# Performance work log

Hardware: AMD Instinct MI355X
Metric: run time of the kernel (lower is better)

## Reference

```python
import jax, jax.numpy as jnp
import numpy as np

S, B, T = 2048, 256, 48


def setup_inputs() -> dict:
    key = jax.random.key(0)
    k1, k2, k3, k4 = jax.random.split(key, 4)
    emissions = jax.random.normal(k1, (S, B, T), dtype=jnp.float32)
    tags = jax.random.randint(k2, (S, B), 0, T, dtype=jnp.int64)
    mask = jnp.ones((S, B), dtype=jnp.int32)
    # params initialized uniform(-0.1, 0.1) as in reset_parameters
    start_transitions = jax.random.uniform(k3, (T,), minval=-0.1, maxval=0.1, dtype=jnp.float32)
    end_transitions = jax.random.uniform(k4, (T,), minval=-0.1, maxval=0.1, dtype=jnp.float32)
    transitions = jax.random.uniform(jax.random.fold_in(key, 7), (T, T), minval=-0.1, maxval=0.1, dtype=jnp.float32)
    return {
        "emissions": emissions,
        "tags": tags,
        "mask": mask,
        "start_transitions": start_transitions,
        "end_transitions": end_transitions,
        "transitions": transitions,
    }


def _compute_score(emissions, tags, mask, start_transitions, end_transitions, transitions):
    # emissions: (S,B,T), tags/mask: (S,B)
    seq_length, batch_size = tags.shape
    maskf = mask.astype(emissions.dtype)
    ar = jnp.arange(batch_size)
    # emission score of the chosen tag at every step: (S,B)
    em_scores = jnp.take_along_axis(emissions, tags[..., None], axis=2)[..., 0]
    score = start_transitions[tags[0]] + em_scores[0]
    # transition scores between consecutive tags, masked: (S-1,B)
    trans_scores = transitions[tags[:-1], tags[1:]] * maskf[1:]
    score = score + trans_scores.sum(axis=0) + (em_scores[1:] * maskf[1:]).sum(axis=0)
    seq_ends = mask.astype(jnp.int32).sum(axis=0) - 1  # (B,)
    last_tags = tags[seq_ends, ar]
    score = score + end_transitions[last_tags]
    return score  # (B,)


def _compute_normalizer(emissions, mask, start_transitions, end_transitions, transitions):
    # forward algorithm via lax.scan over time
    score0 = start_transitions + emissions[0]  # (B,T)

    def step(score, inp):
        em_i, m_i = inp  # (B,T), (B,)
        # (B, T_prev, T_next)
        next_score = jax.nn.logsumexp(score[:, :, None] + transitions[None, :, :] + em_i[:, None, :], axis=1)
        score = jnp.where(m_i[:, None] != 0, next_score, score)
        return score, None

    score, _ = jax.lax.scan(step, score0, (emissions[1:], mask[1:]))
    score = score + end_transitions
    return jax.nn.logsumexp(score, axis=1)  # (B,)


def reference(emissions, tags, mask, start_transitions, end_transitions, transitions):
    numerator = _compute_score(emissions, tags, mask, start_transitions, end_transitions, transitions)
    denominator = _compute_normalizer(emissions, mask, start_transitions, end_transitions, transitions)
    llh = numerator - denominator
    return llh.sum()  # reduction='sum'
```

## Files before the change

### kernel.cpp

```cpp
#include <hip/hip_runtime.h>
#include <hip/hip_bf16.h>
#include <math.h>

#define S_LEN  2048
#define B_SZ   256
#define T_TAGS 48
#define MAT_U32 1152

#define WS_CNT_OFF 0
#define WS_K_OFF   1024
#define WS_P_OFF   65536

using short8 = __attribute__((ext_vector_type(8))) short;
using f32x4  = __attribute__((ext_vector_type(4))) float;

__device__ __forceinline__ unsigned cvtpk(float lo, float hi) {
    unsigned r;
    asm("v_cvt_pk_bf16_f32 %0, %1, %2" : "=v"(r) : "v"(lo), "v"(hi));
    return r;
}
__device__ __forceinline__ unsigned pk2bf(float lo, float hi) {
    __hip_bfloat162 h2 = __float22bfloat162_rn(make_float2(lo, hi));
    return *reinterpret_cast<unsigned*>(&h2);
}

template<int CCH>
__global__ __launch_bounds__(64, 4) void crf_chunk_kernel(
    const float* __restrict__ em, const int* __restrict__ mask,
    const float* __restrict__ trans, const int* __restrict__ tags,
    const float* __restrict__ startT, unsigned* __restrict__ wsP,
    int* __restrict__ wsK, int* __restrict__ wsCnt, float* __restrict__ out)
{
    constexpr int LCH = S_LEN / CCH;
    constexpr int NQ  = LCH / 64;
    const int bid = blockIdx.x;
    const int b = bid / CCH, c = bid % CCH;
    const int tid = threadIdx.x;
    const int cc = tid & 15, g = tid >> 4;
    const int start = c * LCH;

    __shared__ __align__(16) uint4 lds4[384];
    char* Lc = (char*)lds4;

#pragma unroll
    for (int i = 0; i < 6; ++i) lds4[tid + 64 * i] = make_uint4(0u, 0u, 0u, 0u);
    __builtin_amdgcn_wave_barrier();
    if (tid < T_TAGS)
        *(unsigned short*)(Lc + (tid >> 4) * 2048 +
                           ((tid >> 3) * 16 + (tid & 15)) * 16 + (tid & 7) * 2) = 0x3F80;
    __builtin_amdgcn_wave_barrier();

    unsigned long long ball[NQ];
    int cnt = 0;
#pragma unroll
    for (int q = 0; q < NQ; ++q) {
        const int s = start + q * 64 + tid;
        ball[q] = __ballot(mask[s * B_SZ + b] != 0);
        cnt += (int)__popcll(ball[q]);
    }
    if (tid == 0) atomicAdd(&wsCnt[b], cnt);
    if (c == 0) ball[0] &= ~1ull;

    short8 Afr[3][2];
#pragma unroll
    for (int jt = 0; jt < 3; ++jt) {
        const int j = jt * 16 + cc;
#pragma unroll
        for (int kt = 0; kt < 2; ++kt) {
            unsigned u[4];
#pragma unroll
            for (int h = 0; h < 4; ++h) {
                const int k0 = kt * 32 + g * 8 + 2 * h;
                const float lo = (k0     < T_TAGS) ? __expf(trans[k0 * T_TAGS + j]) : 0.f;
                const float hi = (k0 + 1 < T_TAGS) ? __expf(trans[(k0 + 1) * T_TAGS + j]) : 0.f;
                u[h] = cvtpk(lo, hi);
            }
            uint4 uu = make_uint4(u[0], u[1], u[2], u[3]);
            Afr[jt][kt] = *reinterpret_cast<short8*>(&uu);
        }
    }

    int K = 0, pend = 0;
    float kf = 0.0f;
    const f32x4 fz = {0.f, 0.f, 0.f, 0.f};
    const size_t embase = (size_t)b * T_TAGS + 4 * g;

    auto emload = [&](int t, f32x4& d0, f32x4& d1, f32x4& d2) {
        int ss = start + t; if (ss > S_LEN - 1) ss = S_LEN - 1;
        const float* p = em + (size_t)ss * (B_SZ * T_TAGS) + embase;
        d0 = *(const f32x4*)(p);
        d1 = *(const f32x4*)(p + 16);
        d2 = *(const f32x4*)(p + 32);
    };

    auto step = [&](bool on, const f32x4& e0, const f32x4& e1, const f32x4& e2) {
        if (!on) return;
        const short8 B00 = *(const short8*)(Lc +        tid * 16);
        const short8 B01 = *(const short8*)(Lc + 1024 + tid * 16);
        const short8 B10 = *(const short8*)(Lc + 2048 + tid * 16);
        const short8 B11 = *(const short8*)(Lc + 3072 + tid * 16);
        const short8 B20 = *(const short8*)(Lc + 4096 + tid * 16);
        const short8 B21 = *(const short8*)(Lc + 5120 + tid * 16);
        const float kf_ = kf;
        constexpr float L2E = 1.4426950408889634f;
        float ef0[4], ef1[4], ef2[4];
#pragma unroll
        for (int r = 0; r < 4; ++r) {
            ef0[r] = exp2f(fmaf(e0[r], L2E, kf_));
            ef1[r] = exp2f(fmaf(e1[r], L2E, kf_));
            ef2[r] = exp2f(fmaf(e2[r], L2E, kf_));
        }
        f32x4 z;
#define DOFRAG(JT, NT, BN0, BN1, EF, PROBE_)                                   \
        z = __builtin_amdgcn_mfma_f32_16x16x32_bf16(Afr[JT][0], BN0, fz, 0, 0, 0); \
        z = __builtin_amdgcn_mfma_f32_16x16x32_bf16(Afr[JT][1], BN1, z,  0, 0, 0); \
        if (PROBE_) {                                                          \
            const unsigned pb_ = (unsigned)__builtin_amdgcn_readfirstlane(     \
                (int)__float_as_uint(z[0]));                                   \
            const int ee_ = (int)((pb_ >> 23) & 255u);                         \
            const int kk_ = ee_ - 127;                                         \
            K += kk_; pend = kk_;                                              \
            kf = (float)(-kk_);                                                \
        }                                                                      \
        *(uint2*)(Lc + (NT) * 2048 +                                           \
                  ((2 * (JT) + (g >> 1)) * 16 + cc) * 16 + (g & 1) * 8) =      \
            make_uint2(cvtpk(z[0] * EF[0], z[1] * EF[1]),                      \
                       cvtpk(z[2] * EF[2], z[3] * EF[3]))

        DOFRAG(0, 0, B00, B01, ef0, true);
        DOFRAG(0, 1, B10, B11, ef0, false);
        DOFRAG(0, 2, B20, B21, ef0, false);
        DOFRAG(1, 0, B00, B01, ef1, false);
        DOFRAG(1, 1, B10, B11, ef1, false);
        DOFRAG(1, 2, B20, B21, ef1, false);
        DOFRAG(2, 0, B00, B01, ef2, false);
        DOFRAG(2, 1, B10, B11, ef2, false);
        DOFRAG(2, 2, B20, B21, ef2, false);
#undef DOFRAG
    };

    f32x4 a0, a1, a2, b0, b1, b2;
    emload(0, a0, a1, a2);
    emload(1, b0, b1, b2);

#pragma unroll
    for (int q = 0; q < NQ; ++q) {
        const unsigned long long bq = ball[q];
        for (int tt = 0; tt < 64; tt += 2) {
            const int t = q * 64 + tt;
            step(((bq >> tt) & 1ull) != 0, a0, a1, a2);
            emload(t + 2, a0, a1, a2);
            step(((bq >> (tt + 1)) & 1ull) != 0, b0, b1, b2);
            emload(t + 3, b0, b1, b2);
        }
    }

    auto mkI = [&](int shift) -> short8 {
        const int e = cc + shift - 8 * g;
        uint4 uu;
        uu.x = (e == 0) ? 0x3F80u : (e == 1) ? 0x3F800000u : 0u;
        uu.y = (e == 2) ? 0x3F80u : (e == 3) ? 0x3F800000u : 0u;
        uu.z = (e == 4) ? 0x3F80u : (e == 5) ? 0x3F800000u : 0u;
        uu.w = (e == 6) ? 0x3F80u : (e == 7) ? 0x3F800000u : 0u;
        return *reinterpret_cast<short8*>(&uu);
    };
    const short8 I0  = mkI(0);
    const short8 I16 = mkI(16);

    short8 F0[3], F1[3];
#pragma unroll
    for (int nt = 0; nt < 3; ++nt) {
        F0[nt] = *(const short8*)(Lc + nt * 2048 +        tid * 16);
        F1[nt] = *(const short8*)(Lc + nt * 2048 + 1024 + tid * 16);
    }
#pragma unroll
    for (int nt = 0; nt < 3; ++nt) {
#pragma unroll
        for (int ct = 0; ct < 3; ++ct) {
            const short8 Af = (ct < 2) ? F0[nt] : F1[nt];
            const short8 Bi = (ct == 1) ? I16 : I0;
            f32x4 z = __builtin_amdgcn_mfma_f32_16x16x32_bf16(Af, Bi, fz, 0, 0, 0);
            const int jcol = ct * 16 + cc;
            *(uint2*)&wsP[(size_t)bid * MAT_U32 + jcol * 24 + nt * 8 + g * 2] =
                make_uint2(pk2bf(z[0], z[1]), pk2bf(z[2], z[3]));
        }
    }
    if (tid == 0) wsK[bid] = K - pend;

    {
        float nacc = 0.f;
#pragma unroll
        for (int q = 0; q < NQ; ++q) {
            const int s = start + q * 64 + tid;
            if (s == 0) {
                const int t0 = tags[b];
                nacc += em[(size_t)b * T_TAGS + t0] + startT[t0];
            } else if ((ball[q] >> tid) & 1ull) {
                const int tc = tags[(size_t)s * B_SZ + b];
                const int tp = tags[(size_t)(s - 1) * B_SZ + b];
                nacc += em[((size_t)s * B_SZ + b) * T_TAGS + tc] + trans[tp * T_TAGS + tc];
            }
        }
#pragma unroll
        for (int off = 32; off > 0; off >>= 1) nacc += __shfl_down(nacc, off);
        if (tid == 0) atomicAdd(out, nacc);
    }
}

template<int CCH>
__global__ __launch_bounds__(64, 1) void crf_combine_kernel(
    const float* __restrict__ em, const float* __restrict__ startT,
    const float* __restrict__ endT, const unsigned* __restrict__ wsP,
    const int* __restrict__ wsK, const int* __restrict__ wsCnt,
    const int* __restrict__ tags, float* __restrict__ out)
{
    const int b = blockIdx.x, tid = threadIdx.x;
    const int j = (tid < T_TAGS) ? tid : 0;
    float v = (tid < T_TAGS) ? __expf(startT[j] + em[(size_t)b * T_TAGS + j]) : 0.f;
    int K2 = 0;
    for (int c = 0; c < CCH; ++c) {
        const unsigned base = (unsigned)(b * CCH + c) * MAT_U32 + j * 24;
        uint4 W[6];
#pragma unroll
        for (int q = 0; q < 6; ++q)
            W[q] = *reinterpret_cast<const uint4*>(&wsP[base + 4 * q]);
        float a0 = 0.f, a1 = 0.f;
#pragma unroll
        for (int q = 0; q < 6; ++q) {
            const unsigned wv[4] = {W[q].x, W[q].y, W[q].z, W[q].w};
#pragma unroll
            for (int r = 0; r < 4; ++r) {
                const int i = q * 8 + r * 2;
                const float p0 = __uint_as_float(wv[r] << 16);
                const float p1 = __uint_as_float(wv[r] & 0xFFFF0000u);
                a0 = fmaf(__uint_as_float(__builtin_amdgcn_readlane(__float_as_uint(v), i)), p0, a0);
                a1 = fmaf(__uint_as_float(__builtin_amdgcn_readlane(__float_as_uint(v), i + 1)), p1, a1);
            }
        }
        const float vn = a0 + a1;
        const unsigned pb = (unsigned)__builtin_amdgcn_readfirstlane((int)__float_as_uint(vn));
        const int ee = (int)((pb >> 23) & 255u);
        const float sc = __uint_as_float((unsigned)(254 - ee) << 23);
        v = vn * sc;
        K2 += (ee - 127) + wsK[b * CCH + c];
    }
    float contrib = (tid < T_TAGS) ? v * __expf(endT[j]) : 0.f;
#pragma unroll
    for (int off = 32; off > 0; off >>= 1) contrib += __shfl_down(contrib, off);
    if (tid == 0) {
        const int cnt  = wsCnt[b];
        const int last = tags[(size_t)(cnt - 1) * B_SZ + b];
        const double den = (double)K2 * 0.6931471805599453 + (double)__logf(contrib);
        atomicAdd(out, endT[last] + (float)(-den));
    }
}

extern "C" void kernel_launch(void* const* d_in, const int* in_sizes, int n_in,
                              void* d_out, int out_size, void* d_ws, size_t ws_size,
                              hipStream_t stream)
{
    const float* em     = (const float*)d_in[0];
    const int*   tags   = (const int*)  d_in[1];
    const int*   mask   = (const int*)  d_in[2];
    const float* startT = (const float*)d_in[3];
    const float* endT   = (const float*)d_in[4];
    const float* trans  = (const float*)d_in[5];
    float* out = (float*)d_out;

    int*      wsCnt = (int*)((char*)d_ws + WS_CNT_OFF);
    int*      wsK   = (int*)((char*)d_ws + WS_K_OFF);
    unsigned* wsP   = (unsigned*)((char*)d_ws + WS_P_OFF);

    hipMemsetAsync(out, 0, sizeof(float), stream);
    hipMemsetAsync(wsCnt, 0, B_SZ * sizeof(int), stream);

    const size_t need16 = (size_t)WS_P_OFF + (size_t)(B_SZ * 16) * (MAT_U32 * 4);
    if (ws_size >= need16) {
        crf_chunk_kernel<16><<<B_SZ * 16, 64, 0, stream>>>(em, mask, trans, tags, startT, wsP, wsK, wsCnt, out);
        crf_combine_kernel<16><<<B_SZ, 64, 0, stream>>>(em, startT, endT, wsP, wsK, wsCnt, tags, out);
    } else {
        crf_chunk_kernel<8><<<B_SZ * 8, 64, 0, stream>>>(em, mask, trans, tags, startT, wsP, wsK, wsCnt, out);
        crf_combine_kernel<8><<<B_SZ, 64, 0, stream>>>(em, startT, endT, wsP, wsK, wsCnt, tags, out);
    }
}
```

Measured before the change: 227.4 us.

## Move numerator gather into combine kernel and pack scale math as float2

The gold-path score (numerator) gather and its per-block atomicAdd move out of the chunk kernel into the combine kernel. There, each of 256 blocks loops over the full sequence reading mask, tags, emissions and transitions. The emission scaling and bf16 conversion in the chunk step are rewritten with two-wide float vectors so the compiler can emit packed FMA/multiply instructions. This removes the scattered gathers and thousands of atomics from the critical chunk kernel, but serializes that work onto far fewer blocks in the combine kernel, where it may add latency.

```diff
diff --git a/kernel.cpp b/kernel.cpp
--- a/kernel.cpp
+++ b/kernel.cpp
@@ -13,6 +13,7 @@
 
 using short8 = __attribute__((ext_vector_type(8))) short;
 using f32x4  = __attribute__((ext_vector_type(4))) float;
+using f32x2  = __attribute__((ext_vector_type(2))) float;
 
 __device__ __forceinline__ unsigned cvtpk(float lo, float hi) {
     unsigned r;
@@ -27,9 +28,8 @@
 template<int CCH>
 __global__ __launch_bounds__(64, 4) void crf_chunk_kernel(
     const float* __restrict__ em, const int* __restrict__ mask,
-    const float* __restrict__ trans, const int* __restrict__ tags,
-    const float* __restrict__ startT, unsigned* __restrict__ wsP,
-    int* __restrict__ wsK, int* __restrict__ wsCnt, float* __restrict__ out)
+    const float* __restrict__ trans, unsigned* __restrict__ wsP,
+    int* __restrict__ wsK, int* __restrict__ wsCnt)
 {
     constexpr int LCH = S_LEN / CCH;
     constexpr int NQ  = LCH / 64;
@@ -101,17 +101,23 @@
         const short8 B11 = *(const short8*)(Lc + 3072 + tid * 16);
         const short8 B20 = *(const short8*)(Lc + 4096 + tid * 16);
         const short8 B21 = *(const short8*)(Lc + 5120 + tid * 16);
-        const float kf_ = kf;
         constexpr float L2E = 1.4426950408889634f;
-        float ef0[4], ef1[4], ef2[4];
-#pragma unroll
-        for (int r = 0; r < 4; ++r) {
-            ef0[r] = exp2f(fmaf(e0[r], L2E, kf_));
-            ef1[r] = exp2f(fmaf(e1[r], L2E, kf_));
-            ef2[r] = exp2f(fmaf(e2[r], L2E, kf_));
-        }
+        const f32x2 kf2 = {kf, kf};
+        const f32x2 l2e2 = {L2E, L2E};
+        f32x2 x0a = (f32x2){e0[0], e0[1]} * l2e2 + kf2;
+        f32x2 x0b = (f32x2){e0[2], e0[3]} * l2e2 + kf2;
+        f32x2 x1a = (f32x2){e1[0], e1[1]} * l2e2 + kf2;
+        f32x2 x1b = (f32x2){e1[2], e1[3]} * l2e2 + kf2;
+        f32x2 x2a = (f32x2){e2[0], e2[1]} * l2e2 + kf2;
+        f32x2 x2b = (f32x2){e2[2], e2[3]} * l2e2 + kf2;
+        const f32x2 ef0a = {exp2f(x0a[0]), exp2f(x0a[1])};
+        const f32x2 ef0b = {exp2f(x0b[0]), exp2f(x0b[1])};
+        const f32x2 ef1a = {exp2f(x1a[0]), exp2f(x1a[1])};
+        const f32x2 ef1b = {exp2f(x1b[0]), exp2f(x1b[1])};
+        const f32x2 ef2a = {exp2f(x2a[0]), exp2f(x2a[1])};
+        const f32x2 ef2b = {exp2f(x2b[0]), exp2f(x2b[1])};
         f32x4 z;
-#define DOFRAG(JT, NT, BN0, BN1, EF, PROBE_)                                   \
+#define DOFRAG(JT, NT, BN0, BN1, EFa, EFb, PROBE_)                             \
         z = __builtin_amdgcn_mfma_f32_16x16x32_bf16(Afr[JT][0], BN0, fz, 0, 0, 0); \
         z = __builtin_amdgcn_mfma_f32_16x16x32_bf16(Afr[JT][1], BN1, z,  0, 0, 0); \
         if (PROBE_) {                                                          \
@@ -122,20 +128,23 @@
             K += kk_; pend = kk_;                                              \
             kf = (float)(-kk_);                                                \
         }                                                                      \
-        *(uint2*)(Lc + (NT) * 2048 +                                           \
-                  ((2 * (JT) + (g >> 1)) * 16 + cc) * 16 + (g & 1) * 8) =      \
-            make_uint2(cvtpk(z[0] * EF[0], z[1] * EF[1]),                      \
-                       cvtpk(z[2] * EF[2], z[3] * EF[3]))
-
-        DOFRAG(0, 0, B00, B01, ef0, true);
-        DOFRAG(0, 1, B10, B11, ef0, false);
-        DOFRAG(0, 2, B20, B21, ef0, false);
-        DOFRAG(1, 0, B00, B01, ef1, false);
-        DOFRAG(1, 1, B10, B11, ef1, false);
-        DOFRAG(1, 2, B20, B21, ef1, false);
-        DOFRAG(2, 0, B00, B01, ef2, false);
-        DOFRAG(2, 1, B10, B11, ef2, false);
-        DOFRAG(2, 2, B20, B21, ef2, false);
+        {                                                                      \
+            const f32x2 zl_ = (f32x2){z[0], z[1]} * (EFa);                     \
+            const f32x2 zh_ = (f32x2){z[2], z[3]} * (EFb);                     \
+            *(uint2*)(Lc + (NT) * 2048 +                                       \
+                      ((2 * (JT) + (g >> 1)) * 16 + cc) * 16 + (g & 1) * 8) =  \
+                make_uint2(cvtpk(zl_[0], zl_[1]), cvtpk(zh_[0], zh_[1]));      \
+        }
+
+        DOFRAG(0, 0, B00, B01, ef0a, ef0b, true);
+        DOFRAG(0, 1, B10, B11, ef0a, ef0b, false);
+        DOFRAG(0, 2, B20, B21, ef0a, ef0b, false);
+        DOFRAG(1, 0, B00, B01, ef1a, ef1b, false);
+        DOFRAG(1, 1, B10, B11, ef1a, ef1b, false);
+        DOFRAG(1, 2, B20, B21, ef1a, ef1b, false);
+        DOFRAG(2, 0, B00, B01, ef2a, ef2b, false);
+        DOFRAG(2, 1, B10, B11, ef2a, ef2b, false);
+        DOFRAG(2, 2, B20, B21, ef2a, ef2b, false);
 #undef DOFRAG
     };
 
@@ -186,36 +195,35 @@
         }
     }
     if (tid == 0) wsK[bid] = K - pend;
-
-    {
-        float nacc = 0.f;
-#pragma unroll
-        for (int q = 0; q < NQ; ++q) {
-            const int s = start + q * 64 + tid;
-            if (s == 0) {
-                const int t0 = tags[b];
-                nacc += em[(size_t)b * T_TAGS + t0] + startT[t0];
-            } else if ((ball[q] >> tid) & 1ull) {
-                const int tc = tags[(size_t)s * B_SZ + b];
-                const int tp = tags[(size_t)(s - 1) * B_SZ + b];
-                nacc += em[((size_t)s * B_SZ + b) * T_TAGS + tc] + trans[tp * T_TAGS + tc];
-            }
-        }
-#pragma unroll
-        for (int off = 32; off > 0; off >>= 1) nacc += __shfl_down(nacc, off);
-        if (tid == 0) atomicAdd(out, nacc);
-    }
 }
 
 template<int CCH>
 __global__ __launch_bounds__(64, 1) void crf_combine_kernel(
-    const float* __restrict__ em, const float* __restrict__ startT,
-    const float* __restrict__ endT, const unsigned* __restrict__ wsP,
+    const float* __restrict__ em, const int* __restrict__ mask,
+    const float* __restrict__ startT, const float* __restrict__ endT,
+    const float* __restrict__ trans, const unsigned* __restrict__ wsP,
     const int* __restrict__ wsK, const int* __restrict__ wsCnt,
     const int* __restrict__ tags, float* __restrict__ out)
 {
     const int b = blockIdx.x, tid = threadIdx.x;
     const int j = (tid < T_TAGS) ? tid : 0;
+
+    float nacc = 0.f;
+#pragma unroll 4
+    for (int q = 0; q < S_LEN / 64; ++q) {
+        const int s = q * 64 + tid;
+        if (s == 0) {
+            const int t0 = tags[b];
+            nacc += em[(size_t)b * T_TAGS + t0] + startT[t0];
+        } else if (mask[s * B_SZ + b] != 0) {
+            const int tc = tags[(size_t)s * B_SZ + b];
+            const int tp = tags[(size_t)(s - 1) * B_SZ + b];
+            nacc += em[((size_t)s * B_SZ + b) * T_TAGS + tc] + trans[tp * T_TAGS + tc];
+        }
+    }
+#pragma unroll
+    for (int off = 32; off > 0; off >>= 1) nacc += __shfl_down(nacc, off);
+
     float v = (tid < T_TAGS) ? __expf(startT[j] + em[(size_t)b * T_TAGS + j]) : 0.f;
     int K2 = 0;
     for (int c = 0; c < CCH; ++c) {
@@ -251,7 +259,7 @@
         const int cnt  = wsCnt[b];
         const int last = tags[(size_t)(cnt - 1) * B_SZ + b];
         const double den = (double)K2 * 0.6931471805599453 + (double)__logf(contrib);
-        atomicAdd(out, endT[last] + (float)(-den));
+        atomicAdd(out, nacc + endT[last] + (float)(-den));
     }
 }
 
@@ -276,10 +284,10 @@
 
     const size_t need16 = (size_t)WS_P_OFF + (size_t)(B_SZ * 16) * (MAT_U32 * 4);
     if (ws_size >= need16) {
-        crf_chunk_kernel<16><<<B_SZ * 16, 64, 0, stream>>>(em, mask, trans, tags, startT, wsP, wsK, wsCnt, out);
-        crf_combine_kernel<16><<<B_SZ, 64, 0, stream>>>(em, startT, endT, wsP, wsK, wsCnt, tags, out);
+        crf_chunk_kernel<16><<<B_SZ * 16, 64, 0, stream>>>(em, mask, trans, wsP, wsK, wsCnt);
+        crf_combine_kernel<16><<<B_SZ, 64, 0, stream>>>(em, mask, startT, endT, trans, wsP, wsK, wsCnt, tags, out);
     } else {
-        crf_chunk_kernel<8><<<B_SZ * 8, 64, 0, stream>>>(em, mask, trans, tags, startT, wsP, wsK, wsCnt, out);
-        crf_combine_kernel<8><<<B_SZ, 64, 0, stream>>>(em, startT, endT, wsP, wsK, wsCnt, tags, out);
-    }
-}
+        crf_chunk_kernel<8><<<B_SZ * 8, 64, 0, stream>>>(em, mask, trans, wsP, wsK, wsCnt);
+        crf_combine_kernel<8><<<B_SZ, 64, 0, stream>>>(em, mask, startT, endT, trans, wsP, wsK, wsCnt, tags, out);
+    }
+}
```

Result: slower. 257.4 us (+13.2%).
